# Performance work log

Measured on AMD Instinct MI355X. Metric: run time of the kernel, lower is better.

The kernel has to match this reference:

```python
import jax, jax.numpy as jnp
import numpy as np

NUM_HEADS = 8
EPS = 1e-6


def setup_inputs() -> dict:
    key = jax.random.key(0)
    ks = jax.random.split(key, 6)
    B, T, E = 2, 4096, 512
    s = 0.02
    x = jax.random.normal(ks[0], (B, T, E), dtype=jnp.float32)
    Wq = jax.random.normal(ks[1], (E, E), dtype=jnp.float32) * s
    Wk = jax.random.normal(ks[2], (E, E), dtype=jnp.float32) * s
    Wv = jax.random.normal(ks[3], (E, E), dtype=jnp.float32) * s
    Wo = jax.random.normal(ks[4], (E, E), dtype=jnp.float32) * s
    bq = jnp.zeros((E,), jnp.float32)
    bk = jnp.zeros((E,), jnp.float32)
    bv = jnp.zeros((E,), jnp.float32)
    bo = jnp.zeros((E,), jnp.float32)
    return {"x": x, "Wq": Wq, "bq": bq, "Wk": Wk, "bk": bk,
            "Wv": Wv, "bv": bv, "Wo": Wo, "bo": bo}


def _linear(x, W, b):
    # torch nn.Linear: y = x @ W.T + b
    return x @ W.T + b


def _feature_map(x):
    return jax.nn.elu(x) + 1.0


def _linear_attention(x, Wq, bq, Wk, bk, Wv, bv, Wo, bo):
    B, T, E = x.shape
    H = NUM_HEADS
    D = E // H

    def heads(y):  # (B,T,E) -> (T,B,H,D), time-major for scan
        return y.reshape(B, T, H, D).transpose(1, 0, 2, 3)

    q = _feature_map(heads(_linear(x, Wq, bq)))
    k = _feature_map(heads(_linear(x, Wk, bk)))
    v = heads(_linear(x, Wv, bv))

    # Causal linear attention: running KV outer-product state S (B,H,D,D)
    # and running key sum z (B,H,D). Equivalent to the naive
    # cumsum-of-outer-products (B,H,T,D,D) formulation, but O(D^2) state.
    S0 = jnp.zeros((B, H, D, D), x.dtype)
    z0 = jnp.zeros((B, H, D), x.dtype)

    def step(carry, qkv):
        S, z = carry
        qt, kt, vt = qkv  # each (B,H,D)
        S = S + kt[..., :, None] * vt[..., None, :]
        z = z + kt
        num = jnp.einsum('bhd,bhde->bhe', qt, S)
        den = jnp.sum(qt * z, axis=-1) + EPS  # (B,H)
        return (S, z), num / den[..., None]

    _, out = jax.lax.scan(step, (S0, z0), (q, k, v))  # (T,B,H,D)
    out = out.transpose(1, 0, 2, 3).reshape(B, T, E)
    return _linear(out, Wo, bo)


def reference(x, Wq, bq, Wk, bk, Wv, bv, Wo, bo):
    return _linear_attention(x, Wq, bq, Wk, bk, Wv, bv, Wo, bo)
```

## Files before the change

kernel.cpp:

```cpp
#include <hip/hip_runtime.h>
#include <hip/hip_bf16.h>

#define T_SEQ 4096
#define EMB   512
#define NH    8
#define HD    64
#define BATCH 2
#define M_ROWS (BATCH * T_SEQ)
#define NCHUNK 64
#define CS     64
#define BHEADS (BATCH * NH)

using bf16 = __hip_bfloat16;
typedef __attribute__((ext_vector_type(8))) short short8;
typedef __attribute__((ext_vector_type(4))) short short4v;
typedef __attribute__((ext_vector_type(4))) float floatx4;

__device__ __forceinline__ float bs2f(short s) {
    return __uint_as_float(((unsigned)(unsigned short)s) << 16);
}
__device__ __forceinline__ short f2bs(float f) {
    bf16 h = __float2bfloat16(f);
    return *reinterpret_cast<short*>(&h);
}
__device__ __forceinline__ float load_elem(const bf16* p, size_t i) {
    return __bfloat162float(p[i]);
}
__device__ __forceinline__ void stage8(const bf16* g, short* l) {
    *reinterpret_cast<short8*>(l) = *reinterpret_cast<const short8*>(g);
}
__device__ __forceinline__ void stage8(const float* g, short* l) {
    float4 a = *reinterpret_cast<const float4*>(g);
    float4 b = *reinterpret_cast<const float4*>(g + 4);
    short8 v;
    v[0] = f2bs(a.x); v[1] = f2bs(a.y); v[2] = f2bs(a.z); v[3] = f2bs(a.w);
    v[4] = f2bs(b.x); v[5] = f2bs(b.y); v[6] = f2bs(b.z); v[7] = f2bs(b.w);
    *reinterpret_cast<short8*>(l) = v;
}

__device__ __forceinline__ void gload_lds16(const short* g, short* l) {
    __builtin_amdgcn_global_load_lds(
        (const __attribute__((address_space(1))) void*)g,
        (__attribute__((address_space(3))) void*)l, 16, 0, 0);
}

#define LDSTR 72

__device__ __forceinline__ int probe_mode(const void* x) {
    const uint4* p = (const uint4*)x;
    const int tid = threadIdx.x;
    bool bad = false;
    #pragma unroll
    for (int i = 0; i < 2; ++i) {
        uint4 u = p[tid + i * 256];
        const unsigned w[4] = {u.x, u.y, u.z, u.w};
        #pragma unroll
        for (int k = 0; k < 4; ++k) {
            const float f = __uint_as_float(w[k] << 16);
            if (!(fabsf(f) <= 1e9f)) bad = true;
        }
    }
    return __syncthreads_or(bad ? 1 : 0) ? 1 : 0;
}

template <typename T>
__device__ __forceinline__ void convert_body(
    const void* const* in, short* xb, short* Wb, short* bb, int c)
{
    if (c < 524288) {
        stage8((const T*)in[0] + (size_t)c * 8, xb + (size_t)c * 8);
    } else if (c < 655360) {
        const int c2 = c - 524288;
        const int w = c2 >> 15;
        const int off = (c2 & 32767) * 8;
        const T* src = (const T*)in[w == 0 ? 1 : (w == 1 ? 3 : (w == 2 ? 5 : 7))];
        stage8(src + off, Wb + w * 262144 + off);
    } else if (c < 655616) {
        const int c3 = c - 655360;
        const int bsel = c3 >> 6;
        const int off = (c3 & 63) * 8;
        const T* src = (const T*)in[bsel == 0 ? 2 : (bsel == 1 ? 4 : (bsel == 2 ? 6 : 8))];
        stage8(src + off, bb + bsel * 512 + off);
    }
}

__global__ __launch_bounds__(256) void convert_all(
    const void* x, const void* Wq, const void* bq,
    const void* Wk, const void* bk, const void* Wv, const void* bv,
    const void* Wo, const void* bo,
    short* __restrict__ xb, short* __restrict__ Wb, short* __restrict__ bb)
{
    const void* in[9] = {x, Wq, bq, Wk, bk, Wv, bv, Wo, bo};
    const int mode = probe_mode(x);
    const int c = blockIdx.x * 256 + threadIdx.x;
    if (mode) convert_body<float>(in, xb, Wb, bb, c);
    else      convert_body<bf16>(in, xb, Wb, bb, c);
}

__global__ __launch_bounds__(256) void qkv_gemm_dl(
    const short* __restrict__ xb, const short* __restrict__ Wb,
    const short* __restrict__ bb,
    bf16* __restrict__ Qf, bf16* __restrict__ Kf, bf16* __restrict__ Vf)
{
    const int mtile = blockIdx.x;
    const int ntile = blockIdx.y;
    const int which = ntile >> 2;
    const short* W = Wb + (size_t)which * 262144;
    const bf16* bias = (const bf16*)(bb + which * 512);
    bf16* outp = (which == 0) ? Qf : ((which == 1) ? Kf : Vf);
    const int nbase = (ntile & 3) * 128;
    const int mbase = mtile * 128;

    __shared__ short As[128 * 64];
    __shared__ short Bs[128 * 64];

    const int tid  = threadIdx.x;
    const int wave = tid >> 6, lane = tid & 63;
    const int wm = wave >> 1, wn = wave & 1;
    const int lm = lane & 15, quad = lane >> 4;
    const int srow = lane >> 3;
    const int scol = (lane & 7) * 8;

    floatx4 acc[4][4];
    const floatx4 zero = {0.f, 0.f, 0.f, 0.f};
    #pragma unroll
    for (int mt = 0; mt < 4; ++mt)
        #pragma unroll
        for (int nt = 0; nt < 4; ++nt) acc[mt][nt] = zero;

    for (int kt = 0; kt < EMB; kt += 64) {
        #pragma unroll
        for (int j = 0; j < 4; ++j) {
            const int issue = wave * 4 + j;
            const int row = issue * 8 + srow;
            gload_lds16(xb + (size_t)(mbase + row) * EMB + kt + scol,
                        &As[issue * 512]);
            gload_lds16(W  + (size_t)(nbase + row) * EMB + kt + scol,
                        &Bs[issue * 512]);
        }
        __syncthreads();
        #pragma unroll
        for (int ks = 0; ks < 2; ++ks) {
            short8 af[4], bfr[4];
            #pragma unroll
            for (int mt = 0; mt < 4; ++mt)
                af[mt] = *reinterpret_cast<const short8*>(
                    &As[(wm * 64 + mt * 16 + lm) * 64 + ks * 32 + quad * 8]);
            #pragma unroll
            for (int nt = 0; nt < 4; ++nt)
                bfr[nt] = *reinterpret_cast<const short8*>(
                    &Bs[(wn * 64 + nt * 16 + lm) * 64 + ks * 32 + quad * 8]);
            #pragma unroll
            for (int mt = 0; mt < 4; ++mt)
                #pragma unroll
                for (int nt = 0; nt < 4; ++nt)
                    acc[mt][nt] = __builtin_amdgcn_mfma_f32_16x16x32_bf16(
                        af[mt], bfr[nt], acc[mt][nt], 0, 0, 0);
        }
        __syncthreads();
    }

    #pragma unroll
    for (int nt = 0; nt < 4; ++nt) {
        const int col = nbase + wn * 64 + nt * 16 + lm;
        const float bv_ = load_elem(bias, col & 511);
        const int h = col >> 6, d = col & 63;
        #pragma unroll
        for (int mt = 0; mt < 4; ++mt)
            #pragma unroll
            for (int r = 0; r < 4; ++r) {
                const int row = mbase + wm * 64 + mt * 16 + quad * 4 + r;
                const int b = row >> 12, t = row & (T_SEQ - 1);
                float v = acc[mt][nt][r] + bv_;
                if (which != 2) v = (v > 0.f) ? (v + 1.f) : __expf(v);
                outp[(((size_t)(b * NH + h)) * T_SEQ + t) * HD + d] = __float2bfloat16(v);
            }
    }
}

__global__ __launch_bounds__(256) void chunk_kv(
    const bf16* __restrict__ Kf, const bf16* __restrict__ Vf,
    float* __restrict__ KVt, float* __restrict__ ksum)
{
    const int bh = blockIdx.x >> 6;
    const int c  = blockIdx.x & 63;
    __shared__ short Kt[64 * LDSTR];
    __shared__ short Vt[64 * LDSTR];
    const int tid = threadIdx.x;
    const bf16* kp = Kf + ((size_t)bh * T_SEQ + c * CS) * HD;
    const bf16* vp = Vf + ((size_t)bh * T_SEQ + c * CS) * HD;

    #pragma unroll
    for (int j = 0; j < 2; ++j) {
        const int u = j * 256 + tid;
        const int e0 = u * 8;
        const int s = e0 >> 6, d0 = e0 & 63;
        short8 ku = *reinterpret_cast<const short8*>(kp + e0);
        short8 vu = *reinterpret_cast<const short8*>(vp + e0);
        #pragma unroll
        for (int i = 0; i < 8; ++i) {
            Kt[(d0 + i) * LDSTR + s] = ku[i];
            Vt[(d0 + i) * LDSTR + s] = vu[i];
        }
    }
    __syncthreads();

    const int w = tid >> 6, lane = tid & 63;
    const int lm = lane & 15, quad = lane >> 4;

    floatx4 acc[4];
    const floatx4 zero = {0.f, 0.f, 0.f, 0.f};
    #pragma unroll
    for (int nt = 0; nt < 4; ++nt) acc[nt] = zero;

    #pragma unroll
    for (int ks = 0; ks < 2; ++ks) {
        short8 av = *reinterpret_cast<const short8*>(
            &Vt[(w * 16 + lm) * LDSTR + ks * 32 + quad * 8]);
        #pragma unroll
        for (int nt = 0; nt < 4; ++nt) {
            short8 bk = *reinterpret_cast<const short8*>(
                &Kt[(nt * 16 + lm) * LDSTR + ks * 32 + quad * 8]);
            acc[nt] = __builtin_amdgcn_mfma_f32_16x16x32_bf16(av, bk, acc[nt], 0, 0, 0);
        }
    }

    float* kvout = KVt + ((size_t)bh * NCHUNK + c) * 4096;
    #pragma unroll
    for (int nt = 0; nt < 4; ++nt)
        #pragma unroll
        for (int r = 0; r < 4; ++r) {
            const int dv = w * 16 + quad * 4 + r;
            const int dk = nt * 16 + lm;
            kvout[dv * 64 + dk] = acc[nt][r];
        }

    if (tid < 64) {
        float s = 0.f;
        #pragma unroll 8
        for (int t = 0; t < 64; ++t) s += bs2f(Kt[tid * LDSTR + t]);
        ksum[((size_t)bh * NCHUNK + c) * 64 + tid] = s;
    }
}

__global__ __launch_bounds__(256) void prefix_kv(
    float* __restrict__ KVt, float* __restrict__ ksum)
{
    const int bh   = blockIdx.x >> 4;
    const int part = blockIdx.x & 15;
    const int tid  = threadIdx.x;
    const int e    = part * 256 + tid;
    float* base = KVt + (size_t)bh * NCHUNK * 4096 + e;

    float s = 0.f;
    #pragma unroll
    for (int cb = 0; cb < 4; ++cb) {
        float v[16];
        #pragma unroll
        for (int i = 0; i < 16; ++i) v[i] = base[(size_t)(cb * 16 + i) * 4096];
        #pragma unroll
        for (int i = 0; i < 16; ++i) {
            const float tmp = v[i];
            base[(size_t)(cb * 16 + i) * 4096] = s;
            s += tmp;
        }
    }

    if (part == 0 && tid < 64) {
        float* zb = ksum + (size_t)bh * NCHUNK * 64 + tid;
        float z = 0.f;
        #pragma unroll
        for (int cb = 0; cb < 4; ++cb) {
            float v[16];
            #pragma unroll
            for (int i = 0; i < 16; ++i) v[i] = zb[(size_t)(cb * 16 + i) * 64];
            #pragma unroll
            for (int i = 0; i < 16; ++i) {
                const float tmp = v[i];
                zb[(size_t)(cb * 16 + i) * 64] = z;
                z += tmp;
            }
        }
    }
}

__global__ __launch_bounds__(256) void attn_mfma(
    const bf16* __restrict__ Qf, const bf16* __restrict__ Kf,
    const bf16* __restrict__ Vf, const float* __restrict__ KVt,
    const float* __restrict__ ksum, bf16* __restrict__ Of)
{
    const int bh = blockIdx.x >> 6;
    const int c  = blockIdx.x & 63;
    const int b  = bh >> 3, h = bh & 7;

    __shared__ short Qs [64 * LDSTR];
    __shared__ short Ksn[64 * LDSTR];
    __shared__ short Vt [64 * LDSTR];
    __shared__ short Ps [64 * LDSTR];
    __shared__ short St [64 * LDSTR];
    __shared__ float zprev[64];

    const int tid = threadIdx.x;
    const int w = tid >> 6, lane = tid & 63;
    const int lm = lane & 15, quad = lane >> 4;
    const size_t coff = ((size_t)bh * T_SEQ + c * CS) * HD;
    const float* Sp = KVt + ((size_t)bh * NCHUNK + c) * 4096;

    #pragma unroll
    for (int j = 0; j < 2; ++j) {
        const int u  = j * 256 + tid;
        const int e0 = u * 8;
        const int r = e0 >> 6, cc = e0 & 63;
        *reinterpret_cast<short8*>(&Qs [r * LDSTR + cc]) =
            *reinterpret_cast<const short8*>(Qf + coff + e0);
        *reinterpret_cast<short8*>(&Ksn[r * LDSTR + cc]) =
            *reinterpret_cast<const short8*>(Kf + coff + e0);
        short8 vu = *reinterpret_cast<const short8*>(Vf + coff + e0);
        #pragma unroll
        for (int i = 0; i < 8; ++i) Vt[(cc + i) * LDSTR + r] = vu[i];
    }
    #pragma unroll
    for (int j = 0; j < 4; ++j) {
        const int u  = j * 256 + tid;
        const int dv = u >> 4, d0 = (u & 15) * 4;
        const float4 s4 = reinterpret_cast<const float4*>(Sp)[u];
        short4v pk;
        pk[0] = f2bs(s4.x); pk[1] = f2bs(s4.y);
        pk[2] = f2bs(s4.z); pk[3] = f2bs(s4.w);
        *reinterpret_cast<short4v*>(&St[dv * LDSTR + d0]) = pk;
    }
    if (tid < 64) zprev[tid] = ksum[((size_t)bh * NCHUNK + c) * 64 + tid];
    __syncthreads();

    const floatx4 zero = {0.f, 0.f, 0.f, 0.f};
    short8 aq[2];
    #pragma unroll
    for (int ks = 0; ks < 2; ++ks)
        aq[ks] = *reinterpret_cast<const short8*>(
            &Qs[(w * 16 + lm) * LDSTR + ks * 32 + quad * 8]);

    floatx4 pacc[4];
    #pragma unroll
    for (int nt = 0; nt < 4; ++nt) pacc[nt] = zero;
    #pragma unroll
    for (int ks = 0; ks < 2; ++ks)
        #pragma unroll
        for (int nt = 0; nt < 4; ++nt) {
            short8 bk = *reinterpret_cast<const short8*>(
                &Ksn[(nt * 16 + lm) * LDSTR + ks * 32 + quad * 8]);
            pacc[nt] = __builtin_amdgcn_mfma_f32_16x16x32_bf16(aq[ks], bk, pacc[nt], 0, 0, 0);
        }

    float tot[4] = {0.f, 0.f, 0.f, 0.f};
    #pragma unroll
    for (int nt = 0; nt < 4; ++nt)
        #pragma unroll
        for (int r = 0; r < 4; ++r) {
            const int t = w * 16 + quad * 4 + r;
            const int s = nt * 16 + lm;
            const float m = (s <= t) ? pacc[nt][r] : 0.f;
            Ps[t * LDSTR + s] = f2bs(m);
            tot[r] += m;
        }
    #pragma unroll
    for (int r = 0; r < 4; ++r) {
        const int t = w * 16 + quad * 4 + r;
        #pragma unroll
        for (int j = 0; j < 4; ++j) {
            const int d = lm + j * 16;
            tot[r] += bs2f(Qs[t * LDSTR + d]) * zprev[d];
        }
    }
    #pragma unroll
    for (int mask = 1; mask < 16; mask <<= 1)
        #pragma unroll
        for (int r = 0; r < 4; ++r) tot[r] += __shfl_xor(tot[r], mask);
    float rdenl[4];
    #pragma unroll
    for (int r = 0; r < 4; ++r) rdenl[r] = 1.f / (tot[r] + 1e-6f);

    floatx4 oacc[4];
    #pragma unroll
    for (int nt = 0; nt < 4; ++nt) oacc[nt] = zero;
    #pragma unroll
    for (int ks = 0; ks < 2; ++ks)
        #pragma unroll
        for (int nt = 0; nt < 4; ++nt) {
            short8 bs = *reinterpret_cast<const short8*>(
                &St[(nt * 16 + lm) * LDSTR + ks * 32 + quad * 8]);
            oacc[nt] = __builtin_amdgcn_mfma_f32_16x16x32_bf16(aq[ks], bs, oacc[nt], 0, 0, 0);
        }
    __syncthreads();

    #pragma unroll
    for (int ks = 0; ks < 2; ++ks) {
        short8 ap = *reinterpret_cast<const short8*>(
            &Ps[(w * 16 + lm) * LDSTR + ks * 32 + quad * 8]);
        #pragma unroll
        for (int nt = 0; nt < 4; ++nt) {
            short8 bv = *reinterpret_cast<const short8*>(
                &Vt[(nt * 16 + lm) * LDSTR + ks * 32 + quad * 8]);
            oacc[nt] = __builtin_amdgcn_mfma_f32_16x16x32_bf16(ap, bv, oacc[nt], 0, 0, 0);
        }
    }

    #pragma unroll
    for (int nt = 0; nt < 4; ++nt)
        #pragma unroll
        for (int r = 0; r < 4; ++r) {
            const int t  = w * 16 + quad * 4 + r;
            const int dv = nt * 16 + lm;
            const int tg = c * CS + t;
            Of[((size_t)(b * T_SEQ + tg)) * EMB + h * HD + dv] =
                __float2bfloat16(oacc[nt][r] * rdenl[r]);
        }
}

__global__ __launch_bounds__(256) void out_proj_dl(
    const void* __restrict__ xprobe,
    const short* __restrict__ A, const short* __restrict__ Wb,
    const short* __restrict__ bb, void* __restrict__ out)
{
    const int mode = probe_mode(xprobe);

    const int mbase = blockIdx.x * 128;
    const int nbase = blockIdx.y * 128;
    const short* W = Wb + (size_t)3 * 262144;
    const bf16* bias = (const bf16*)(bb + 3 * 512);

    __shared__ short As[128 * 64];
    __shared__ short Bs[128 * 64];

    const int tid  = threadIdx.x;
    const int wave = tid >> 6, lane = tid & 63;
    const int wm = wave >> 1, wn = wave & 1;
    const int lm = lane & 15, quad = lane >> 4;
    const int srow = lane >> 3;
    const int scol = (lane & 7) * 8;

    floatx4 acc[4][4];
    const floatx4 zero = {0.f, 0.f, 0.f, 0.f};
    #pragma unroll
    for (int mt = 0; mt < 4; ++mt)
        #pragma unroll
        for (int nt = 0; nt < 4; ++nt) acc[mt][nt] = zero;

    for (int kt = 0; kt < EMB; kt += 64) {
        #pragma unroll
        for (int j = 0; j < 4; ++j) {
            const int issue = wave * 4 + j;
            const int row = issue * 8 + srow;
            gload_lds16(A + (size_t)(mbase + row) * EMB + kt + scol,
                        &As[issue * 512]);
            gload_lds16(W + (size_t)(nbase + row) * EMB + kt + scol,
                        &Bs[issue * 512]);
        }
        __syncthreads();
        #pragma unroll
        for (int ks = 0; ks < 2; ++ks) {
            short8 af[4], bfr[4];
            #pragma unroll
            for (int mt = 0; mt < 4; ++mt)
                af[mt] = *reinterpret_cast<const short8*>(
                    &As[(wm * 64 + mt * 16 + lm) * 64 + ks * 32 + quad * 8]);
            #pragma unroll
            for (int nt = 0; nt < 4; ++nt)
                bfr[nt] = *reinterpret_cast<const short8*>(
                    &Bs[(wn * 64 + nt * 16 + lm) * 64 + ks * 32 + quad * 8]);
            #pragma unroll
            for (int mt = 0; mt < 4; ++mt)
                #pragma unroll
                for (int nt = 0; nt < 4; ++nt)
                    acc[mt][nt] = __builtin_amdgcn_mfma_f32_16x16x32_bf16(
                        af[mt], bfr[nt], acc[mt][nt], 0, 0, 0);
        }
        __syncthreads();
    }

    #pragma unroll
    for (int nt = 0; nt < 4; ++nt) {
        const int col = nbase + wn * 64 + nt * 16 + lm;
        const float bv_ = load_elem(bias, col);
        #pragma unroll
        for (int mt = 0; mt < 4; ++mt)
            #pragma unroll
            for (int r = 0; r < 4; ++r) {
                const int row = mbase + wm * 64 + mt * 16 + quad * 4 + r;
                const float v = acc[mt][nt][r] + bv_;
                if (mode) ((float*)out)[(size_t)row * EMB + col] = v;
                else      ((bf16*)out)[(size_t)row * EMB + col] = __float2bfloat16(v);
            }
    }
}

extern "C" void kernel_launch(void* const* d_in, const int* in_sizes, int n_in,
                              void* d_out, int out_size, void* d_ws, size_t ws_size,
                              hipStream_t stream)
{
    bf16* Qf = (bf16*)((char*)d_ws + 64);
    bf16* Kf = Qf + 4194304;
    bf16* Vf = Kf + 4194304;
    float* KVt = (float*)(Vf + 4194304);
    short* xb = (short*)KVt;
    float* ks = KVt + 4194304;
    bf16* Of = (bf16*)(ks + 65536);
    short* Wb = (short*)(Of + 4194304);
    short* bb = Wb + 1048576;

    convert_all<<<dim3(2561), 256, 0, stream>>>(
        d_in[0], d_in[1], d_in[2], d_in[3], d_in[4],
        d_in[5], d_in[6], d_in[7], d_in[8], xb, Wb, bb);

    qkv_gemm_dl<<<dim3(64, 12), 256, 0, stream>>>(xb, Wb, bb, Qf, Kf, Vf);
    chunk_kv<<<dim3(BHEADS * NCHUNK), 256, 0, stream>>>(Kf, Vf, KVt, ks);
    prefix_kv<<<dim3(BHEADS * 16), 256, 0, stream>>>(KVt, ks);
    attn_mfma<<<dim3(BHEADS * NCHUNK), 256, 0, stream>>>(Qf, Kf, Vf, KVt, ks, Of);

    out_proj_dl<<<dim3(64, 4), 256, 0, stream>>>(
        d_in[0], (const short*)Of, Wb, bb, d_out);
}
```

Baseline: 161.6 us.

## Store chunk KV state in bf16 and read MFMA operands directly from global

chunk_kv now writes the per-chunk KV state as bf16 instead of fp32 and also writes a transposed V tile to global memory. prefix_kv scans the bf16 state, accumulating in fp32 but storing bf16 prefixes. The attention kernel drops most of its LDS staging and loads Q, K, transposed V and the state fragments straight from global, and it computes the q·z denominator term with a shuffle reduction. This cuts fp32 state traffic, LDS transposes and a barrier, but adds an extra V write, uncoalesced fragment loads from global, and bf16 rounding of the running prefix sums.

Measured after the change: 164.7 us. Within noise of the previous version (+1.9%).

```diff
diff --git a/kernel.cpp b/kernel.cpp
--- a/kernel.cpp
+++ b/kernel.cpp
@@ -13,7 +13,6 @@
 
 using bf16 = __hip_bfloat16;
 typedef __attribute__((ext_vector_type(8))) short short8;
-typedef __attribute__((ext_vector_type(4))) short short4v;
 typedef __attribute__((ext_vector_type(4))) float floatx4;
 
 __device__ __forceinline__ float bs2f(short s) {
@@ -180,7 +179,8 @@
 
 __global__ __launch_bounds__(256) void chunk_kv(
     const bf16* __restrict__ Kf, const bf16* __restrict__ Vf,
-    float* __restrict__ KVt, float* __restrict__ ksum)
+    short* __restrict__ KVc, float* __restrict__ ksum,
+    short* __restrict__ Vtg)
 {
     const int bh = blockIdx.x >> 6;
     const int c  = blockIdx.x & 63;
@@ -189,6 +189,7 @@
     const int tid = threadIdx.x;
     const bf16* kp = Kf + ((size_t)bh * T_SEQ + c * CS) * HD;
     const bf16* vp = Vf + ((size_t)bh * T_SEQ + c * CS) * HD;
+    const size_t toff = ((size_t)bh * NCHUNK + c) * 4096;
 
     #pragma unroll
     for (int j = 0; j < 2; ++j) {
@@ -205,6 +206,15 @@
     }
     __syncthreads();
 
+    #pragma unroll
+    for (int j = 0; j < 2; ++j) {
+        const int u = j * 256 + tid;
+        const int e0 = u * 8;
+        const int row = e0 >> 6, col = e0 & 63;
+        *reinterpret_cast<short8*>(Vtg + toff + row * 64 + col) =
+            *reinterpret_cast<const short8*>(&Vt[row * LDSTR + col]);
+    }
+
     const int w = tid >> 6, lane = tid & 63;
     const int lm = lane & 15, quad = lane >> 4;
 
@@ -225,14 +235,13 @@
         }
     }
 
-    float* kvout = KVt + ((size_t)bh * NCHUNK + c) * 4096;
     #pragma unroll
     for (int nt = 0; nt < 4; ++nt)
         #pragma unroll
         for (int r = 0; r < 4; ++r) {
             const int dv = w * 16 + quad * 4 + r;
             const int dk = nt * 16 + lm;
-            kvout[dv * 64 + dk] = acc[nt][r];
+            KVc[toff + dv * 64 + dk] = f2bs(acc[nt][r]);
         }
 
     if (tid < 64) {
@@ -244,24 +253,24 @@
 }
 
 __global__ __launch_bounds__(256) void prefix_kv(
-    float* __restrict__ KVt, float* __restrict__ ksum)
+    short* __restrict__ KVc, float* __restrict__ ksum)
 {
     const int bh   = blockIdx.x >> 4;
     const int part = blockIdx.x & 15;
     const int tid  = threadIdx.x;
     const int e    = part * 256 + tid;
-    float* base = KVt + (size_t)bh * NCHUNK * 4096 + e;
+    short* base = KVc + (size_t)bh * NCHUNK * 4096 + e;
 
     float s = 0.f;
     #pragma unroll
     for (int cb = 0; cb < 4; ++cb) {
         float v[16];
         #pragma unroll
-        for (int i = 0; i < 16; ++i) v[i] = base[(size_t)(cb * 16 + i) * 4096];
+        for (int i = 0; i < 16; ++i) v[i] = bs2f(base[(size_t)(cb * 16 + i) * 4096]);
         #pragma unroll
         for (int i = 0; i < 16; ++i) {
             const float tmp = v[i];
-            base[(size_t)(cb * 16 + i) * 4096] = s;
+            base[(size_t)(cb * 16 + i) * 4096] = f2bs(s);
             s += tmp;
         }
     }
@@ -284,61 +293,46 @@
     }
 }
 
-__global__ __launch_bounds__(256) void attn_mfma(
+__global__ __launch_bounds__(256) void attn_lite(
     const bf16* __restrict__ Qf, const bf16* __restrict__ Kf,
-    const bf16* __restrict__ Vf, const float* __restrict__ KVt,
+    const short* __restrict__ Vtg, const short* __restrict__ KVc,
     const float* __restrict__ ksum, bf16* __restrict__ Of)
 {
     const int bh = blockIdx.x >> 6;
     const int c  = blockIdx.x & 63;
     const int b  = bh >> 3, h = bh & 7;
 
-    __shared__ short Qs [64 * LDSTR];
-    __shared__ short Ksn[64 * LDSTR];
-    __shared__ short Vt [64 * LDSTR];
-    __shared__ short Ps [64 * LDSTR];
-    __shared__ short St [64 * LDSTR];
-    __shared__ float zprev[64];
+    __shared__ short Ps[64 * LDSTR];
+    __shared__ float qzbuf[64];
 
     const int tid = threadIdx.x;
     const int w = tid >> 6, lane = tid & 63;
     const int lm = lane & 15, quad = lane >> 4;
     const size_t coff = ((size_t)bh * T_SEQ + c * CS) * HD;
-    const float* Sp = KVt + ((size_t)bh * NCHUNK + c) * 4096;
-
-    #pragma unroll
-    for (int j = 0; j < 2; ++j) {
-        const int u  = j * 256 + tid;
-        const int e0 = u * 8;
-        const int r = e0 >> 6, cc = e0 & 63;
-        *reinterpret_cast<short8*>(&Qs [r * LDSTR + cc]) =
-            *reinterpret_cast<const short8*>(Qf + coff + e0);
-        *reinterpret_cast<short8*>(&Ksn[r * LDSTR + cc]) =
-            *reinterpret_cast<const short8*>(Kf + coff + e0);
-        short8 vu = *reinterpret_cast<const short8*>(Vf + coff + e0);
-        #pragma unroll
-        for (int i = 0; i < 8; ++i) Vt[(cc + i) * LDSTR + r] = vu[i];
-    }
-    #pragma unroll
-    for (int j = 0; j < 4; ++j) {
-        const int u  = j * 256 + tid;
-        const int dv = u >> 4, d0 = (u & 15) * 4;
-        const float4 s4 = reinterpret_cast<const float4*>(Sp)[u];
-        short4v pk;
-        pk[0] = f2bs(s4.x); pk[1] = f2bs(s4.y);
-        pk[2] = f2bs(s4.z); pk[3] = f2bs(s4.w);
-        *reinterpret_cast<short4v*>(&St[dv * LDSTR + d0]) = pk;
-    }
-    if (tid < 64) zprev[tid] = ksum[((size_t)bh * NCHUNK + c) * 64 + tid];
-    __syncthreads();
-
-    const floatx4 zero = {0.f, 0.f, 0.f, 0.f};
+    const size_t toff = ((size_t)bh * NCHUNK + c) * 4096;
+
     short8 aq[2];
     #pragma unroll
     for (int ks = 0; ks < 2; ++ks)
         aq[ks] = *reinterpret_cast<const short8*>(
-            &Qs[(w * 16 + lm) * LDSTR + ks * 32 + quad * 8]);
-
+            Qf + coff + (w * 16 + lm) * HD + ks * 32 + quad * 8);
+
+    const float* zp = ksum + ((size_t)bh * NCHUNK + c) * 64;
+    float qz = 0.f;
+    #pragma unroll
+    for (int ks = 0; ks < 2; ++ks) {
+        const float4 z0 = *reinterpret_cast<const float4*>(zp + ks * 32 + quad * 8);
+        const float4 z1 = *reinterpret_cast<const float4*>(zp + ks * 32 + quad * 8 + 4);
+        qz += bs2f(aq[ks][0]) * z0.x + bs2f(aq[ks][1]) * z0.y
+            + bs2f(aq[ks][2]) * z0.z + bs2f(aq[ks][3]) * z0.w
+            + bs2f(aq[ks][4]) * z1.x + bs2f(aq[ks][5]) * z1.y
+            + bs2f(aq[ks][6]) * z1.z + bs2f(aq[ks][7]) * z1.w;
+    }
+    qz += __shfl_xor(qz, 16);
+    qz += __shfl_xor(qz, 32);
+    if (quad == 0) qzbuf[w * 16 + lm] = qz;
+
+    const floatx4 zero = {0.f, 0.f, 0.f, 0.f};
     floatx4 pacc[4];
     #pragma unroll
     for (int nt = 0; nt < 4; ++nt) pacc[nt] = zero;
@@ -347,7 +341,7 @@
         #pragma unroll
         for (int nt = 0; nt < 4; ++nt) {
             short8 bk = *reinterpret_cast<const short8*>(
-                &Ksn[(nt * 16 + lm) * LDSTR + ks * 32 + quad * 8]);
+                Kf + coff + (nt * 16 + lm) * HD + ks * 32 + quad * 8);
             pacc[nt] = __builtin_amdgcn_mfma_f32_16x16x32_bf16(aq[ks], bk, pacc[nt], 0, 0, 0);
         }
 
@@ -363,21 +357,9 @@
             tot[r] += m;
         }
     #pragma unroll
-    for (int r = 0; r < 4; ++r) {
-        const int t = w * 16 + quad * 4 + r;
-        #pragma unroll
-        for (int j = 0; j < 4; ++j) {
-            const int d = lm + j * 16;
-            tot[r] += bs2f(Qs[t * LDSTR + d]) * zprev[d];
-        }
-    }
-    #pragma unroll
     for (int mask = 1; mask < 16; mask <<= 1)
         #pragma unroll
         for (int r = 0; r < 4; ++r) tot[r] += __shfl_xor(tot[r], mask);
-    float rdenl[4];
-    #pragma unroll
-    for (int r = 0; r < 4; ++r) rdenl[r] = 1.f / (tot[r] + 1e-6f);
 
     floatx4 oacc[4];
     #pragma unroll
@@ -387,10 +369,9 @@
         #pragma unroll
         for (int nt = 0; nt < 4; ++nt) {
             short8 bs = *reinterpret_cast<const short8*>(
-                &St[(nt * 16 + lm) * LDSTR + ks * 32 + quad * 8]);
+                KVc + toff + (nt * 16 + lm) * 64 + ks * 32 + quad * 8);
             oacc[nt] = __builtin_amdgcn_mfma_f32_16x16x32_bf16(aq[ks], bs, oacc[nt], 0, 0, 0);
         }
-    __syncthreads();
 
     #pragma unroll
     for (int ks = 0; ks < 2; ++ks) {
@@ -399,10 +380,15 @@
         #pragma unroll
         for (int nt = 0; nt < 4; ++nt) {
             short8 bv = *reinterpret_cast<const short8*>(
-                &Vt[(nt * 16 + lm) * LDSTR + ks * 32 + quad * 8]);
+                Vtg + toff + (nt * 16 + lm) * 64 + ks * 32 + quad * 8);
             oacc[nt] = __builtin_amdgcn_mfma_f32_16x16x32_bf16(ap, bv, oacc[nt], 0, 0, 0);
         }
     }
+
+    float rdenl[4];
+    #pragma unroll
+    for (int r = 0; r < 4; ++r)
+        rdenl[r] = 1.f / (tot[r] + qzbuf[w * 16 + quad * 4 + r] + 1e-6f);
 
     #pragma unroll
     for (int nt = 0; nt < 4; ++nt)
@@ -500,21 +486,22 @@
     bf16* Qf = (bf16*)((char*)d_ws + 64);
     bf16* Kf = Qf + 4194304;
     bf16* Vf = Kf + 4194304;
-    float* KVt = (float*)(Vf + 4194304);
-    short* xb = (short*)KVt;
-    float* ks = KVt + 4194304;
+    short* KVc = (short*)(Vf + 4194304);
+    short* xb = KVc;
+    float* ks = (float*)(KVc + 4194304);
     bf16* Of = (bf16*)(ks + 65536);
     short* Wb = (short*)(Of + 4194304);
     short* bb = Wb + 1048576;
+    short* Vtg = bb + 2048;
 
     convert_all<<<dim3(2561), 256, 0, stream>>>(
         d_in[0], d_in[1], d_in[2], d_in[3], d_in[4],
         d_in[5], d_in[6], d_in[7], d_in[8], xb, Wb, bb);
 
     qkv_gemm_dl<<<dim3(64, 12), 256, 0, stream>>>(xb, Wb, bb, Qf, Kf, Vf);
-    chunk_kv<<<dim3(BHEADS * NCHUNK), 256, 0, stream>>>(Kf, Vf, KVt, ks);
-    prefix_kv<<<dim3(BHEADS * 16), 256, 0, stream>>>(KVt, ks);
-    attn_mfma<<<dim3(BHEADS * NCHUNK), 256, 0, stream>>>(Qf, Kf, Vf, KVt, ks, Of);
+    chunk_kv<<<dim3(BHEADS * NCHUNK), 256, 0, stream>>>(Kf, Vf, KVc, ks, Vtg);
+    prefix_kv<<<dim3(BHEADS * 16), 256, 0, stream>>>(KVc, ks);
+    attn_lite<<<dim3(BHEADS * NCHUNK), 256, 0, stream>>>(Qf, Kf, Vtg, KVc, ks, Of);
 
     out_proj_dl<<<dim3(64, 4), 256, 0, stream>>>(
         d_in[0], (const short*)Of, Wb, bb, d_out);
```
